# Optimization experiments

Hardware: AMD Instinct MI355X
Metric: run time of the kernel (lower is better)

The kernel has to match this reference:

```python
import jax, jax.numpy as jnp
import numpy as np

B, S, D, H, E = 2, 2048, 1024, 2048, 8
TOP_K = 2
AUX_COEF = 0.01


def setup_inputs() -> dict:
    key = jax.random.key(0)
    ks = jax.random.split(key, 5)
    x = jax.random.normal(ks[0], (B, S, D), jnp.float32)
    Wr = jax.random.normal(ks[1], (E, D), jnp.float32) * 0.02   # router: Linear(D, E) weight [E, D]
    W1 = jax.random.normal(ks[2], (E, H, D), jnp.float32) * 0.02  # per-expert Linear(D, H)
    W2 = jax.random.normal(ks[3], (E, D, H), jnp.float32) * 0.02  # per-expert Linear(H, D)
    W3 = jax.random.normal(ks[4], (E, H, D), jnp.float32) * 0.02  # per-expert Linear(D, H)
    return {"x": x, "Wr": Wr, "W1": W1, "W2": W2, "W3": W3}


def reference(x, Wr, W1, W2, W3):
    b, s, d = x.shape
    e = Wr.shape[0]
    xf = x.reshape(-1, d)                               # [N, D]
    logits = xf @ Wr.T                                  # [N, E]
    probs = jax.nn.softmax(logits, axis=-1)
    _, topk_idx = jax.lax.top_k(logits, TOP_K)          # indices from logits (as in torch code)
    topk_probs, _ = jax.lax.top_k(probs, TOP_K)         # values from probs (same order; softmax monotone)
    # aux loss: density of top-1 expert * mean router prob
    density = jnp.mean(jax.nn.one_hot(topk_idx[:, 0], e, dtype=xf.dtype), axis=0)
    aux_loss = AUX_COEF * jnp.sum(density * probs.mean(axis=0)) * e
    # combine gates: gate[n, j] = sum_i topk_probs[n,i] * 1[topk_idx[n,i]==j]
    gates = jnp.sum(jax.nn.one_hot(topk_idx, e, dtype=xf.dtype) * topk_probs[..., None], axis=1)  # [N, E]
    # dense per-expert SwiGLU; masked combine gives identical math to gather/scatter loop
    h = jax.nn.silu(jnp.einsum('nd,ehd->enh', xf, W1)) * jnp.einsum('nd,ehd->enh', xf, W3)  # [E, N, H]
    y = jnp.einsum('enh,edh->end', h, W2)               # [E, N, D]
    out = jnp.einsum('ne,end->nd', gates, y)            # [N, D]
    return out.reshape(b, s, d), aux_loss
```

## Files before the change

### kernel.cpp

```cpp
#include <hip/hip_runtime.h>
#include <stdint.h>

#define NTOK 4096
#define DD 1024
#define HH 2048
#define NE 8
#define CAP 4096

typedef short bf16x8 __attribute__((ext_vector_type(8)));
typedef float f32x4 __attribute__((ext_vector_type(4)));
typedef unsigned short u16;
typedef unsigned int u32;

__device__ __forceinline__ u16 f2b(float f){
    union { float f; u32 u; } v; v.f = f;
    return (u16)((v.u + 0x7fffu + ((v.u >> 16) & 1u)) >> 16);
}
__device__ __forceinline__ float b2f(u16 h){
    union { u32 u; float f; } v; v.u = ((u32)h) << 16;
    return v.f;
}
__device__ __forceinline__ u32 pk2(float a, float b){
    return (u32)f2b(a) | ((u32)f2b(b) << 16);
}
__device__ __forceinline__ void gload16(const u16* g, u16* l){
    __builtin_amdgcn_global_load_lds((const __attribute__((address_space(1))) u32*)g,
                                     (__attribute__((address_space(3))) u32*)l, 16, 0, 0);
}
__device__ __forceinline__ int prefix_off(const int* __restrict__ cnt, int e){
    int o = 0;
    #pragma unroll
    for (int i = 0; i < NE; ++i) if (i < e) o += cnt[i];
    return o;
}

__global__ __launch_bounds__(256) void prep_kernel(const float* __restrict__ x,
        const float* __restrict__ Wr,
        const float* __restrict__ W1, const float* __restrict__ W2, const float* __restrict__ W3,
        u16* __restrict__ xb, u16* __restrict__ w1b, u16* __restrict__ w2b, u16* __restrict__ w3b,
        int* __restrict__ cnt, int* __restrict__ list,
        float* __restrict__ glist, float* __restrict__ psum,
        int* __restrict__ cnt1, int* __restrict__ islot){
    __shared__ float wS[NE * DD];
    __shared__ float psumS[NE];
    __shared__ int cnt1S[NE], cntS[NE], baseS[NE];
    __shared__ int tE[32], tL[32];
    __shared__ float tP[32];
    int tid = threadIdx.x;
    int bid = blockIdx.x;

    if (bid >= 256){
        int cb = bid - 256;
        int m = cb >> 10, blk = cb & 1023;
        const float* s = (m == 0) ? W1 : (m == 1) ? W2 : W3;
        u16* d = (m == 0) ? w1b : (m == 1) ? w2b : w3b;
        int base = blk * 4096 + tid;
        #pragma unroll 4
        for (int j = 0; j < 16; ++j){
            int i = base + j * 256;
            float4 v = reinterpret_cast<const float4*>(s)[i];
            ushort4 o; o.x = f2b(v.x); o.y = f2b(v.y); o.z = f2b(v.z); o.w = f2b(v.w);
            reinterpret_cast<ushort4*>(d)[i] = o;
        }
        return;
    }

    for (int i = tid; i < NE * DD / 4; i += 256)
        reinterpret_cast<float4*>(wS)[i] = reinterpret_cast<const float4*>(Wr)[i];
    if (tid < NE){ psumS[tid] = 0.f; cnt1S[tid] = 0; cntS[tid] = 0; }
    __syncthreads();
    int lane = tid & 63, w = tid >> 6;
    for (int t = 0; t < 4; ++t){
        int li = w * 4 + t;
        int n = bid * 16 + li;
        const float4* xr = reinterpret_cast<const float4*>(x + (size_t)n * DD);
        ushort4* xbr = reinterpret_cast<ushort4*>(xb + (size_t)n * DD);
        float acc[NE];
        #pragma unroll
        for (int e = 0; e < NE; ++e) acc[e] = 0.f;
        #pragma unroll
        for (int j = 0; j < 4; ++j){
            float4 xv = xr[lane + 64 * j];
            ushort4 xo; xo.x = f2b(xv.x); xo.y = f2b(xv.y); xo.z = f2b(xv.z); xo.w = f2b(xv.w);
            xbr[lane + 64 * j] = xo;
            #pragma unroll
            for (int e = 0; e < NE; ++e){
                float4 wv = reinterpret_cast<const float4*>(wS + e * DD)[lane + 64 * j];
                acc[e] += xv.x * wv.x + xv.y * wv.y + xv.z * wv.z + xv.w * wv.w;
            }
        }
        #pragma unroll
        for (int e = 0; e < NE; ++e){
            float v = acc[e];
            #pragma unroll
            for (int s = 32; s > 0; s >>= 1) v += __shfl_xor(v, s);
            acc[e] = v;
        }
        if (lane == 0){
            float mx = acc[0];
            #pragma unroll
            for (int e = 1; e < NE; ++e) mx = fmaxf(mx, acc[e]);
            float p[NE], sm = 0.f;
            #pragma unroll
            for (int e = 0; e < NE; ++e){ p[e] = expf(acc[e] - mx); sm += p[e]; }
            float inv = 1.f / sm;
            #pragma unroll
            for (int e = 0; e < NE; ++e){ p[e] *= inv; atomicAdd(&psumS[e], p[e]); }
            int i0 = 0;
            #pragma unroll
            for (int e = 1; e < NE; ++e) if (acc[e] > acc[i0]) i0 = e;
            int i1 = -1;
            #pragma unroll
            for (int e = 0; e < NE; ++e) if (e != i0 && (i1 < 0 || acc[e] > acc[i1])) i1 = e;
            atomicAdd(&cnt1S[i0], 1);
            int l0 = atomicAdd(&cntS[i0], 1);
            int l1 = atomicAdd(&cntS[i1], 1);
            tE[li * 2] = i0; tE[li * 2 + 1] = i1;
            tP[li * 2] = p[i0]; tP[li * 2 + 1] = p[i1];
            tL[li * 2] = l0; tL[li * 2 + 1] = l1;
        }
    }
    __syncthreads();
    if (tid < NE){
        baseS[tid] = atomicAdd(&cnt[tid], cntS[tid]);
        atomicAdd(&psum[tid], psumS[tid]);
        atomicAdd(&cnt1[tid], cnt1S[tid]);
    }
    __syncthreads();
    if (tid < 32){
        int e = tE[tid], pos = baseS[e] + tL[tid];
        int n = bid * 16 + (tid >> 1);
        list[e * CAP + pos]  = n;
        glist[e * CAP + pos] = tP[tid];
        islot[n * 2 + (tid & 1)] = e * CAP + pos;
    }
}

__global__ __launch_bounds__(256, 3) void ffn1_kernel(const u16* __restrict__ xb,
        const u16* __restrict__ w1b, const u16* __restrict__ w3b,
        const int* __restrict__ cnt, const int* __restrict__ list,
        u16* __restrict__ hbuf){
    int bid = blockIdx.x;
    int e = bid & 7;
    int slot = bid >> 3;
    int rows = cnt[e];
    int hoff = prefix_off(cnt, e);
    int n0 = (slot & 31) * 64;

    __shared__ u16 aS[128 * 64];
    __shared__ u16 bS[128 * 64];

    int tid = threadIdx.x, lane = tid & 63, w = tid >> 6;
    int wm = (w & 1) * 64, wn = (w >> 1) * 32;
    int fr = lane & 15, fg = lane >> 4, fr7 = fr & 7;
    int rc = lane >> 3, ce = ((lane & 7) ^ rc) * 8;

    const u16* bptr[4];
    #pragma unroll
    for (int q = 0; q < 4; ++q){
        int br = (w * 4 + q) * 8 + rc;
        const u16* wb = (br < 64) ? w1b : w3b;
        bptr[q] = wb + ((size_t)e * HH + n0 + (br & 63)) * DD + ce;
    }
    u16* aL = aS + w * 4 * 512;
    u16* bL = bS + w * 4 * 512;

    for (int mt = slot >> 5; mt < 32; mt += 3){
        int m0 = mt << 7;
        if (m0 >= rows) break;

        const u16* aptr[4];
        #pragma unroll
        for (int q = 0; q < 4; ++q){
            int r = m0 + (w * 4 + q) * 8 + rc;
            int tok = list[e * CAP + (r < rows ? r : rows - 1)];
            aptr[q] = xb + (size_t)tok * DD + ce;
        }

        f32x4 acc1[4][2], acc3[4][2];
        #pragma unroll
        for (int mi = 0; mi < 4; ++mi)
            #pragma unroll
            for (int ni = 0; ni < 2; ++ni)
                #pragma unroll
                for (int j = 0; j < 4; ++j){ acc1[mi][ni][j] = 0.f; acc3[mi][ni][j] = 0.f; }

        for (int k0 = 0; k0 < DD; k0 += 64){
            #pragma unroll
            for (int q = 0; q < 4; ++q){
                gload16(aptr[q] + k0, aL + q * 512);
                gload16(bptr[q] + k0, bL + q * 512);
            }
            __syncthreads();
            #pragma unroll
            for (int ks = 0; ks < 2; ++ks){
                int sl = ((ks * 4 + fg) ^ fr7) * 8;
                bf16x8 a[4], b1[2], b3[2];
                #pragma unroll
                for (int mi = 0; mi < 4; ++mi)
                    a[mi] = *reinterpret_cast<const bf16x8*>(&aS[(wm + mi * 16 + fr) * 64 + sl]);
                #pragma unroll
                for (int ni = 0; ni < 2; ++ni){
                    b1[ni] = *reinterpret_cast<const bf16x8*>(&bS[(wn + ni * 16 + fr) * 64 + sl]);
                    b3[ni] = *reinterpret_cast<const bf16x8*>(&bS[(64 + wn + ni * 16 + fr) * 64 + sl]);
                }
                #pragma unroll
                for (int mi = 0; mi < 4; ++mi)
                    #pragma unroll
                    for (int ni = 0; ni < 2; ++ni){
                        acc1[mi][ni] = __builtin_amdgcn_mfma_f32_16x16x32_bf16(a[mi], b1[ni], acc1[mi][ni], 0, 0, 0);
                        acc3[mi][ni] = __builtin_amdgcn_mfma_f32_16x16x32_bf16(a[mi], b3[ni], acc3[mi][ni], 0, 0, 0);
                    }
            }
            __syncthreads();
        }

        #pragma unroll
        for (int mi = 0; mi < 4; ++mi)
            #pragma unroll
            for (int ni = 0; ni < 2; ++ni)
                #pragma unroll
                for (int j = 0; j < 4; ++j){
                    int r = wm + mi * 16 + fg * 4 + j;
                    int tr = m0 + r;
                    if (tr < rows){
                        int c = n0 + wn + ni * 16 + fr;
                        float v1 = acc1[mi][ni][j], v3 = acc3[mi][ni][j];
                        float hv = (v1 / (1.f + expf(-v1))) * v3;
                        hbuf[(size_t)(hoff + tr) * HH + c] = f2b(hv);
                    }
                }
    }
}

__global__ __launch_bounds__(256, 3) void ffn2_kernel(const u16* __restrict__ hbuf,
        const u16* __restrict__ w2b, const int* __restrict__ cnt,
        u16* __restrict__ ybuf){
    int bid = blockIdx.x;
    int widx = (bid & 7) * 256 + (bid >> 3);
    int e = widx >> 8, n0t = (widx >> 5) & 7, mt = widx & 31;
    int rows = cnt[e];
    int m0 = mt * 128;
    if (m0 >= rows) return;
    int n0 = n0t * 128;
    int hoff = prefix_off(cnt, e);

    __shared__ u16 aS[128 * 64];
    __shared__ u16 bS[128 * 64];

    int tid = threadIdx.x, lane = tid & 63, w = tid >> 6;
    int wm = (w & 1) * 64, wn = (w >> 1) * 64;
    int fr = lane & 15, fg = lane >> 4, fr7 = fr & 7;
    int rc = lane >> 3, ce = ((lane & 7) ^ rc) * 8;

    const u16* aptr[4];
    #pragma unroll
    for (int q = 0; q < 4; ++q){
        int r = m0 + (w * 4 + q) * 8 + rc;
        if (r >= rows) r = rows - 1;
        aptr[q] = hbuf + (size_t)(hoff + r) * HH + ce;
    }
    const u16* bp = w2b + ((size_t)e * DD + n0 + w * 32 + rc) * HH + ce;
    u16* aL = aS + w * 4 * 512;
    u16* bL = bS + w * 4 * 512;

    f32x4 acc[4][4];
    #pragma unroll
    for (int mi = 0; mi < 4; ++mi)
        #pragma unroll
        for (int ni = 0; ni < 4; ++ni)
            #pragma unroll
            for (int j = 0; j < 4; ++j) acc[mi][ni][j] = 0.f;

    for (int k0 = 0; k0 < HH; k0 += 64){
        #pragma unroll
        for (int q = 0; q < 4; ++q){
            gload16(aptr[q] + k0, aL + q * 512);
            gload16(bp + q * 8 * HH + k0, bL + q * 512);
        }
        __syncthreads();
        #pragma unroll
        for (int ks = 0; ks < 2; ++ks){
            int sl = ((ks * 4 + fg) ^ fr7) * 8;
            bf16x8 a[4], b[4];
            #pragma unroll
            for (int mi = 0; mi < 4; ++mi)
                a[mi] = *reinterpret_cast<const bf16x8*>(&aS[(wm + mi * 16 + fr) * 64 + sl]);
            #pragma unroll
            for (int ni = 0; ni < 4; ++ni)
                b[ni] = *reinterpret_cast<const bf16x8*>(&bS[(wn + ni * 16 + fr) * 64 + sl]);
            #pragma unroll
            for (int mi = 0; mi < 4; ++mi)
                #pragma unroll
                for (int ni = 0; ni < 4; ++ni)
                    acc[mi][ni] = __builtin_amdgcn_mfma_f32_16x16x32_bf16(a[mi], b[ni], acc[mi][ni], 0, 0, 0);
        }
        __syncthreads();
    }

    #pragma unroll
    for (int mi = 0; mi < 4; ++mi)
        #pragma unroll
        for (int ni = 0; ni < 4; ++ni)
            #pragma unroll
            for (int j = 0; j < 4; ++j){
                int r = wm + mi * 16 + fg * 4 + j;
                int tr = m0 + r;
                if (tr < rows){
                    int c = wn + ni * 16 + fr;
                    ybuf[(size_t)(hoff + tr) * DD + n0 + c] = f2b(acc[mi][ni][j]);
                }
            }
}

__global__ __launch_bounds__(256, 2) void ffn1_small(const u16* __restrict__ xb,
        const float* __restrict__ W1f, const float* __restrict__ W3f,
        const int* __restrict__ cnt, const int* __restrict__ list,
        u16* __restrict__ hbuf){
    int bid = blockIdx.x;
    int widx = (bid & 7) * 512 + (bid >> 3);
    int e = widx >> 9, n0t = (widx >> 5) & 15, mt = widx & 31;
    int rows = cnt[e];
    int m0 = mt * 128;
    if (m0 >= rows) return;
    int n0 = n0t * 128;
    int hoff = prefix_off(cnt, e);
    __shared__ u16 aS[128 * 64];
    __shared__ u16 b1S[128 * 64];
    __shared__ u16 b3S[128 * 64];
    int tid = threadIdx.x, lane = tid & 63, w = tid >> 6;
    int wm = (w & 1) * 64, wn = (w >> 1) * 64;
    int fr = lane & 15, fg = lane >> 4, fr7 = fr & 7;
    int rc = lane >> 3, ce = ((lane & 7) ^ rc) * 8;
    const u16* aptr[4];
    #pragma unroll
    for (int q = 0; q < 4; ++q){
        int r = m0 + (w * 4 + q) * 8 + rc;
        int tok = list[e * CAP + (r < rows ? r : rows - 1)];
        aptr[q] = xb + (size_t)tok * DD + ce;
    }
    size_t brw = (size_t)(e * HH + n0 + w * 32 + rc) * DD + ce;
    const float* b1pf = W1f + brw;
    const float* b3pf = W3f + brw;
    u16* aL  = aS  + w * 4 * 512;
    u16* b1L = b1S + w * 4 * 512;
    u16* b3L = b3S + w * 4 * 512;
    f32x4 acc1[4][4], acc3[4][4];
    #pragma unroll
    for (int mi = 0; mi < 4; ++mi)
        #pragma unroll
        for (int ni = 0; ni < 4; ++ni)
            #pragma unroll
            for (int j = 0; j < 4; ++j){ acc1[mi][ni][j] = 0.f; acc3[mi][ni][j] = 0.f; }
    for (int k0 = 0; k0 < DD; k0 += 64){
        #pragma unroll
        for (int q = 0; q < 4; ++q){
            gload16(aptr[q] + k0, aL + q * 512);
            const float* s1 = b1pf + q * 8 * DD + k0;
            float4 f0 = reinterpret_cast<const float4*>(s1)[0];
            float4 f1 = reinterpret_cast<const float4*>(s1)[1];
            int4 v; v.x = pk2(f0.x,f0.y); v.y = pk2(f0.z,f0.w); v.z = pk2(f1.x,f1.y); v.w = pk2(f1.z,f1.w);
            *reinterpret_cast<int4*>(b1L + q * 512 + lane * 8) = v;
            const float* s3 = b3pf + q * 8 * DD + k0;
            float4 g0 = reinterpret_cast<const float4*>(s3)[0];
            float4 g1 = reinterpret_cast<const float4*>(s3)[1];
            int4 u; u.x = pk2(g0.x,g0.y); u.y = pk2(g0.z,g0.w); u.z = pk2(g1.x,g1.y); u.w = pk2(g1.z,g1.w);
            *reinterpret_cast<int4*>(b3L + q * 512 + lane * 8) = u;
        }
        __syncthreads();
        #pragma unroll
        for (int ks = 0; ks < 2; ++ks){
            int sl = ((ks * 4 + fg) ^ fr7) * 8;
            bf16x8 a[4], b1[4], b3[4];
            #pragma unroll
            for (int mi = 0; mi < 4; ++mi)
                a[mi] = *reinterpret_cast<const bf16x8*>(&aS[(wm + mi * 16 + fr) * 64 + sl]);
            #pragma unroll
            for (int ni = 0; ni < 4; ++ni){
                b1[ni] = *reinterpret_cast<const bf16x8*>(&b1S[(wn + ni * 16 + fr) * 64 + sl]);
                b3[ni] = *reinterpret_cast<const bf16x8*>(&b3S[(wn + ni * 16 + fr) * 64 + sl]);
            }
            #pragma unroll
            for (int mi = 0; mi < 4; ++mi)
                #pragma unroll
                for (int ni = 0; ni < 4; ++ni){
                    acc1[mi][ni] = __builtin_amdgcn_mfma_f32_16x16x32_bf16(a[mi], b1[ni], acc1[mi][ni], 0, 0, 0);
                    acc3[mi][ni] = __builtin_amdgcn_mfma_f32_16x16x32_bf16(a[mi], b3[ni], acc3[mi][ni], 0, 0, 0);
                }
        }
        __syncthreads();
    }
    #pragma unroll
    for (int mi = 0; mi < 4; ++mi)
        #pragma unroll
        for (int ni = 0; ni < 4; ++ni)
            #pragma unroll
            for (int j = 0; j < 4; ++j){
                int r = wm + mi * 16 + fg * 4 + j;
                int tr = m0 + r;
                if (tr < rows){
                    int c = wn + ni * 16 + fr;
                    float v1 = acc1[mi][ni][j], v3 = acc3[mi][ni][j];
                    float hv = (v1 / (1.f + expf(-v1))) * v3;
                    hbuf[(size_t)(hoff + tr) * HH + n0 + c] = f2b(hv);
                }
            }
}

__global__ __launch_bounds__(256, 2) void ffn2_small(const u16* __restrict__ hbuf,
        const float* __restrict__ W2f, const int* __restrict__ cnt,
        u16* __restrict__ ybuf){
    int bid = blockIdx.x;
    int widx = (bid & 7) * 256 + (bid >> 3);
    int e = widx >> 8, n0t = (widx >> 5) & 7, mt = widx & 31;
    int rows = cnt[e];
    int m0 = mt * 128;
    if (m0 >= rows) return;
    int n0 = n0t * 128;
    int hoff = prefix_off(cnt, e);
    __shared__ u16 aS[128 * 64];
    __shared__ u16 bS[128 * 64];
    int tid = threadIdx.x, lane = tid & 63, w = tid >> 6;
    int wm = (w & 1) * 64, wn = (w >> 1) * 64;
    int fr = lane & 15, fg = lane >> 4, fr7 = fr & 7;
    int rc = lane >> 3, ce = ((lane & 7) ^ rc) * 8;
    const u16* aptr[4];
    #pragma unroll
    for (int q = 0; q < 4; ++q){
        int r = m0 + (w * 4 + q) * 8 + rc;
        if (r >= rows) r = rows - 1;
        aptr[q] = hbuf + (size_t)(hoff + r) * HH + ce;
    }
    const float* b2pf = W2f + (size_t)(e * DD + n0 + w * 32 + rc) * HH + ce;
    u16* aL = aS + w * 4 * 512;
    u16* bL = bS + w * 4 * 512;
    f32x4 acc[4][4];
    #pragma unroll
    for (int mi = 0; mi < 4; ++mi)
        #pragma unroll
        for (int ni = 0; ni < 4; ++ni)
            #pragma unroll
            for (int j = 0; j < 4; ++j) acc[mi][ni][j] = 0.f;
    for (int k0 = 0; k0 < HH; k0 += 64){
        #pragma unroll
        for (int q = 0; q < 4; ++q){
            gload16(aptr[q] + k0, aL + q * 512);
            const float* s2 = b2pf + q * 8 * HH + k0;
            float4 f0 = reinterpret_cast<const float4*>(s2)[0];
            float4 f1 = reinterpret_cast<const float4*>(s2)[1];
            int4 v; v.x = pk2(f0.x,f0.y); v.y = pk2(f0.z,f0.w); v.z = pk2(f1.x,f1.y); v.w = pk2(f1.z,f1.w);
            *reinterpret_cast<int4*>(bL + q * 512 + lane * 8) = v;
        }
        __syncthreads();
        #pragma unroll
        for (int ks = 0; ks < 2; ++ks){
            int sl = ((ks * 4 + fg) ^ fr7) * 8;
            bf16x8 a[4], b[4];
            #pragma unroll
            for (int mi = 0; mi < 4; ++mi)
                a[mi] = *reinterpret_cast<const bf16x8*>(&aS[(wm + mi * 16 + fr) * 64 + sl]);
            #pragma unroll
            for (int ni = 0; ni < 4; ++ni)
                b[ni] = *reinterpret_cast<const bf16x8*>(&bS[(wn + ni * 16 + fr) * 64 + sl]);
            #pragma unroll
            for (int mi = 0; mi < 4; ++mi)
                #pragma unroll
                for (int ni = 0; ni < 4; ++ni)
                    acc[mi][ni] = __builtin_amdgcn_mfma_f32_16x16x32_bf16(a[mi], b[ni], acc[mi][ni], 0, 0, 0);
        }
        __syncthreads();
    }
    #pragma unroll
    for (int mi = 0; mi < 4; ++mi)
        #pragma unroll
        for (int ni = 0; ni < 4; ++ni)
            #pragma unroll
            for (int j = 0; j < 4; ++j){
                int r = wm + mi * 16 + fg * 4 + j;
                int tr = m0 + r;
                if (tr < rows){
                    int c = wn + ni * 16 + fr;
                    ybuf[(size_t)(hoff + tr) * DD + n0 + c] = f2b(acc[mi][ni][j]);
                }
            }
}

__global__ __launch_bounds__(256) void combine_kernel(const u16* __restrict__ ybuf,
        const int* __restrict__ islot, const int* __restrict__ cnt,
        const float* __restrict__ glist, const float* __restrict__ psum,
        const int* __restrict__ cnt1, float* __restrict__ out){
    int idx = blockIdx.x * 256 + threadIdx.x;
    if (idx == 0){
        float aux = 0.f;
        #pragma unroll
        for (int e = 0; e < NE; ++e)
            aux += ((float)cnt1[e] * (1.f / NTOK)) * (psum[e] * (1.f / NTOK));
        out[(size_t)NTOK * DD] = 0.01f * aux * (float)NE;
    }
    int n = idx >> 7, c = (idx & 127) * 8;
    int id0 = islot[n * 2], id1 = islot[n * 2 + 1];
    int r0 = prefix_off(cnt, id0 >> 12) + (id0 & 4095);
    int r1 = prefix_off(cnt, id1 >> 12) + (id1 & 4095);
    float g0 = glist[id0], g1 = glist[id1];
    ushort4 y0a = reinterpret_cast<const ushort4*>(ybuf + (size_t)r0 * DD + c)[0];
    ushort4 y0b = reinterpret_cast<const ushort4*>(ybuf + (size_t)r0 * DD + c)[1];
    ushort4 y1a = reinterpret_cast<const ushort4*>(ybuf + (size_t)r1 * DD + c)[0];
    ushort4 y1b = reinterpret_cast<const ushort4*>(ybuf + (size_t)r1 * DD + c)[1];
    float4 o0, o1;
    o0.x = g0 * b2f(y0a.x) + g1 * b2f(y1a.x);
    o0.y = g0 * b2f(y0a.y) + g1 * b2f(y1a.y);
    o0.z = g0 * b2f(y0a.z) + g1 * b2f(y1a.z);
    o0.w = g0 * b2f(y0a.w) + g1 * b2f(y1a.w);
    o1.x = g0 * b2f(y0b.x) + g1 * b2f(y1b.x);
    o1.y = g0 * b2f(y0b.y) + g1 * b2f(y1b.y);
    o1.z = g0 * b2f(y0b.z) + g1 * b2f(y1b.z);
    o1.w = g0 * b2f(y0b.w) + g1 * b2f(y1b.w);
    float4* op = reinterpret_cast<float4*>(out + (size_t)n * DD + c);
    op[0] = o0; op[1] = o1;
}

extern "C" void kernel_launch(void* const* d_in, const int* in_sizes, int n_in,
                              void* d_out, int out_size, void* d_ws, size_t ws_size,
                              hipStream_t stream) {
    const float* x  = (const float*)d_in[0];
    const float* Wr = (const float*)d_in[1];
    const float* W1 = (const float*)d_in[2];
    const float* W2 = (const float*)d_in[3];
    const float* W3 = (const float*)d_in[4];
    float* out = (float*)d_out;

    char* wp = (char*)d_ws;
    u16*   hbuf  = (u16*)  (wp);
    u16*   xb    = (u16*)  (wp + 33554432);
    int*   list  = (int*)  (wp + 41943040);
    float* glist = (float*)(wp + 42074112);
    int*   cnt   = (int*)  (wp + 42205184);
    float* psum  = (float*)(wp + 42205216);
    int*   cnt1  = (int*)  (wp + 42205248);
    int*   islot = (int*)  (wp + 42205312);
    const size_t WOFF = 42238208;
    const size_t WB   = 33554432;
    u16* w1b = (u16*)(wp + WOFF);
    u16* w2b = (u16*)(wp + WOFF + WB);
    u16* w3b = (u16*)(wp + WOFF + 2 * WB);
    u16* ybuf = (u16*)(wp + WOFF);
    const size_t NEED_FULL = WOFF + 3 * WB;
    bool bw = ws_size >= NEED_FULL;

    hipMemsetAsync(wp + 42205184, 0, 128, stream);

    prep_kernel<<<bw ? 3328 : 256, 256, 0, stream>>>(
        x, Wr, W1, W2, W3, xb, w1b, w2b, w3b, cnt, list, glist, psum, cnt1, islot);
    if (bw){
        ffn1_kernel<<<768, 256, 0, stream>>>(xb, w1b, w3b, cnt, list, hbuf);
        ffn2_kernel<<<2048, 256, 0, stream>>>(hbuf, w2b, cnt, ybuf);
    } else {
        ffn1_small<<<4096, 256, 0, stream>>>(xb, W1, W3, cnt, list, hbuf);
        ffn2_small<<<2048, 256, 0, stream>>>(hbuf, W2, cnt, ybuf);
    }
    combine_kernel<<<NTOK * (DD / 8) / 256, 256, 0, stream>>>(
        ybuf, islot, cnt, glist, psum, cnt1, out);
}
```

Baseline: 209.5 us.

## Overlap W2 bf16 conversion with FFN1 and make FFN2 persistent

Moves the fp32-to-bf16 conversion of W2 out of the prep kernel and into extra blocks of the FFN1 launch, so that bandwidth-bound conversion can run alongside the FFN1 GEMM. FFN2 changes from one block per (expert, n-tile, m-tile) with early exits to 768 persistent blocks that loop over m-tiles with stride 12. The intent is to shorten the critical path and cut wasted block launches. The risk is that conversion blocks compete with GEMM blocks for CUs and memory bandwidth, and the fixed stride may load-balance poorly when expert counts are skewed.

```diff
diff --git a/kernel.cpp b/kernel.cpp
--- a/kernel.cpp
+++ b/kernel.cpp
@@ -36,8 +36,8 @@
 
 __global__ __launch_bounds__(256) void prep_kernel(const float* __restrict__ x,
         const float* __restrict__ Wr,
-        const float* __restrict__ W1, const float* __restrict__ W2, const float* __restrict__ W3,
-        u16* __restrict__ xb, u16* __restrict__ w1b, u16* __restrict__ w2b, u16* __restrict__ w3b,
+        const float* __restrict__ W1, const float* __restrict__ W3,
+        u16* __restrict__ xb, u16* __restrict__ w1b, u16* __restrict__ w3b,
         int* __restrict__ cnt, int* __restrict__ list,
         float* __restrict__ glist, float* __restrict__ psum,
         int* __restrict__ cnt1, int* __restrict__ islot){
@@ -52,8 +52,8 @@
     if (bid >= 256){
         int cb = bid - 256;
         int m = cb >> 10, blk = cb & 1023;
-        const float* s = (m == 0) ? W1 : (m == 1) ? W2 : W3;
-        u16* d = (m == 0) ? w1b : (m == 1) ? w2b : w3b;
+        const float* s = (m == 0) ? W1 : W3;
+        u16* d = (m == 0) ? w1b : w3b;
         int base = blk * 4096 + tid;
         #pragma unroll 4
         for (int j = 0; j < 16; ++j){
@@ -138,9 +138,25 @@
 
 __global__ __launch_bounds__(256, 3) void ffn1_kernel(const u16* __restrict__ xb,
         const u16* __restrict__ w1b, const u16* __restrict__ w3b,
+        const float* __restrict__ W2f, u16* __restrict__ w2b,
         const int* __restrict__ cnt, const int* __restrict__ list,
         u16* __restrict__ hbuf){
     int bid = blockIdx.x;
+    int tid = threadIdx.x;
+
+    if (bid >= 768){
+        int cb = bid - 768;
+        int base = cb * 4096 + tid;
+        #pragma unroll 4
+        for (int j = 0; j < 16; ++j){
+            int i = base + j * 256;
+            float4 v = reinterpret_cast<const float4*>(W2f)[i];
+            ushort4 o; o.x = f2b(v.x); o.y = f2b(v.y); o.z = f2b(v.z); o.w = f2b(v.w);
+            reinterpret_cast<ushort4*>(w2b)[i] = o;
+        }
+        return;
+    }
+
     int e = bid & 7;
     int slot = bid >> 3;
     int rows = cnt[e];
@@ -150,7 +166,7 @@
     __shared__ u16 aS[128 * 64];
     __shared__ u16 bS[128 * 64];
 
-    int tid = threadIdx.x, lane = tid & 63, w = tid >> 6;
+    int lane = tid & 63, w = tid >> 6;
     int wm = (w & 1) * 64, wn = (w >> 1) * 32;
     int fr = lane & 15, fg = lane >> 4, fr7 = fr & 7;
     int rc = lane >> 3, ce = ((lane & 7) ^ rc) * 8;
@@ -237,13 +253,11 @@
         const u16* __restrict__ w2b, const int* __restrict__ cnt,
         u16* __restrict__ ybuf){
     int bid = blockIdx.x;
-    int widx = (bid & 7) * 256 + (bid >> 3);
-    int e = widx >> 8, n0t = (widx >> 5) & 7, mt = widx & 31;
+    int e = bid & 7;
+    int slot = bid >> 3;
     int rows = cnt[e];
-    int m0 = mt * 128;
-    if (m0 >= rows) return;
-    int n0 = n0t * 128;
     int hoff = prefix_off(cnt, e);
+    int n0 = (slot & 7) * 128;
 
     __shared__ u16 aS[128 * 64];
     __shared__ u16 bS[128 * 64];
@@ -253,64 +267,70 @@
     int fr = lane & 15, fg = lane >> 4, fr7 = fr & 7;
     int rc = lane >> 3, ce = ((lane & 7) ^ rc) * 8;
 
-    const u16* aptr[4];
-    #pragma unroll
-    for (int q = 0; q < 4; ++q){
-        int r = m0 + (w * 4 + q) * 8 + rc;
-        if (r >= rows) r = rows - 1;
-        aptr[q] = hbuf + (size_t)(hoff + r) * HH + ce;
-    }
     const u16* bp = w2b + ((size_t)e * DD + n0 + w * 32 + rc) * HH + ce;
     u16* aL = aS + w * 4 * 512;
     u16* bL = bS + w * 4 * 512;
 
-    f32x4 acc[4][4];
-    #pragma unroll
-    for (int mi = 0; mi < 4; ++mi)
-        #pragma unroll
-        for (int ni = 0; ni < 4; ++ni)
-            #pragma unroll
-            for (int j = 0; j < 4; ++j) acc[mi][ni][j] = 0.f;
-
-    for (int k0 = 0; k0 < HH; k0 += 64){
+    for (int mt = slot >> 3; mt < 32; mt += 12){
+        int m0 = mt << 7;
+        if (m0 >= rows) break;
+
+        const u16* aptr[4];
         #pragma unroll
         for (int q = 0; q < 4; ++q){
-            gload16(aptr[q] + k0, aL + q * 512);
-            gload16(bp + q * 8 * HH + k0, bL + q * 512);
-        }
-        __syncthreads();
-        #pragma unroll
-        for (int ks = 0; ks < 2; ++ks){
-            int sl = ((ks * 4 + fg) ^ fr7) * 8;
-            bf16x8 a[4], b[4];
-            #pragma unroll
-            for (int mi = 0; mi < 4; ++mi)
-                a[mi] = *reinterpret_cast<const bf16x8*>(&aS[(wm + mi * 16 + fr) * 64 + sl]);
+            int r = m0 + (w * 4 + q) * 8 + rc;
+            if (r >= rows) r = rows - 1;
+            aptr[q] = hbuf + (size_t)(hoff + r) * HH + ce;
+        }
+
+        f32x4 acc[4][4];
+        #pragma unroll
+        for (int mi = 0; mi < 4; ++mi)
             #pragma unroll
             for (int ni = 0; ni < 4; ++ni)
-                b[ni] = *reinterpret_cast<const bf16x8*>(&bS[(wn + ni * 16 + fr) * 64 + sl]);
-            #pragma unroll
-            for (int mi = 0; mi < 4; ++mi)
+                #pragma unroll
+                for (int j = 0; j < 4; ++j) acc[mi][ni][j] = 0.f;
+
+        for (int k0 = 0; k0 < HH; k0 += 64){
+            #pragma unroll
+            for (int q = 0; q < 4; ++q){
+                gload16(aptr[q] + k0, aL + q * 512);
+                gload16(bp + q * 8 * HH + k0, bL + q * 512);
+            }
+            __syncthreads();
+            #pragma unroll
+            for (int ks = 0; ks < 2; ++ks){
+                int sl = ((ks * 4 + fg) ^ fr7) * 8;
+                bf16x8 a[4], b[4];
+                #pragma unroll
+                for (int mi = 0; mi < 4; ++mi)
+                    a[mi] = *reinterpret_cast<const bf16x8*>(&aS[(wm + mi * 16 + fr) * 64 + sl]);
                 #pragma unroll
                 for (int ni = 0; ni < 4; ++ni)
-                    acc[mi][ni] = __builtin_amdgcn_mfma_f32_16x16x32_bf16(a[mi], b[ni], acc[mi][ni], 0, 0, 0);
-        }
-        __syncthreads();
-    }
-
-    #pragma unroll
-    for (int mi = 0; mi < 4; ++mi)
-        #pragma unroll
-        for (int ni = 0; ni < 4; ++ni)
-            #pragma unroll
-            for (int j = 0; j < 4; ++j){
-                int r = wm + mi * 16 + fg * 4 + j;
-                int tr = m0 + r;
-                if (tr < rows){
-                    int c = wn + ni * 16 + fr;
-                    ybuf[(size_t)(hoff + tr) * DD + n0 + c] = f2b(acc[mi][ni][j]);
+                    b[ni] = *reinterpret_cast<const bf16x8*>(&bS[(wn + ni * 16 + fr) * 64 + sl]);
+                #pragma unroll
+                for (int mi = 0; mi < 4; ++mi)
+                    #pragma unroll
+                    for (int ni = 0; ni < 4; ++ni)
+                        acc[mi][ni] = __builtin_amdgcn_mfma_f32_16x16x32_bf16(a[mi], b[ni], acc[mi][ni], 0, 0, 0);
+            }
+            __syncthreads();
+        }
+
+        #pragma unroll
+        for (int mi = 0; mi < 4; ++mi)
+            #pragma unroll
+            for (int ni = 0; ni < 4; ++ni)
+                #pragma unroll
+                for (int j = 0; j < 4; ++j){
+                    int r = wm + mi * 16 + fg * 4 + j;
+                    int tr = m0 + r;
+                    if (tr < rows){
+                        int c = wn + ni * 16 + fr;
+                        ybuf[(size_t)(hoff + tr) * DD + n0 + c] = f2b(acc[mi][ni][j]);
+                    }
                 }
-            }
+    }
 }
 
 __global__ __launch_bounds__(256, 2) void ffn1_small(const u16* __restrict__ xb,
@@ -549,11 +569,11 @@
 
     hipMemsetAsync(wp + 42205184, 0, 128, stream);
 
-    prep_kernel<<<bw ? 3328 : 256, 256, 0, stream>>>(
-        x, Wr, W1, W2, W3, xb, w1b, w2b, w3b, cnt, list, glist, psum, cnt1, islot);
+    prep_kernel<<<bw ? 2304 : 256, 256, 0, stream>>>(
+        x, Wr, W1, W3, xb, w1b, w3b, cnt, list, glist, psum, cnt1, islot);
     if (bw){
-        ffn1_kernel<<<768, 256, 0, stream>>>(xb, w1b, w3b, cnt, list, hbuf);
-        ffn2_kernel<<<2048, 256, 0, stream>>>(hbuf, w2b, cnt, ybuf);
+        ffn1_kernel<<<1792, 256, 0, stream>>>(xb, w1b, w3b, W2, w2b, cnt, list, hbuf);
+        ffn2_kernel<<<768, 256, 0, stream>>>(hbuf, w2b, cnt, ybuf);
     } else {
         ffn1_small<<<4096, 256, 0, stream>>>(xb, W1, W3, cnt, list, hbuf);
         ffn2_small<<<2048, 256, 0, stream>>>(hbuf, W2, cnt, ybuf);
```

Result: faster. 196.6 us (median of 2 runs) (-6.2%).
